# Kernel optimization log

Measured on AMD Instinct MI355X. Metric: run time of the kernel, lower is better.

## Reference

```python
import jax, jax.numpy as jnp
import numpy as np
from jax import lax

# Static hyperparameters of preprocess_proposals (typical BARON config values)
SHAPE_RATIO_THR = 0.25
AREA_RATIO_THR = 0.01
OBJECTNESS_THR = 0.85
NMS_THR = 0.3
EPS_UNION = 1e-6   # mmdet bbox_overlaps eps
EPS_RATIO = 1e-12
IMG_SIZE = 1024.0
N = 8192


def setup_inputs() -> dict:
    key = jax.random.key(0)
    k1, k2, k3 = jax.random.split(key, 3)
    # realistic proposals inside a 1024x1024 image
    centers = jax.random.uniform(k1, (N, 2), minval=0.0, maxval=IMG_SIZE)
    wh = jax.random.uniform(k2, (N, 2), minval=16.0, maxval=512.0)
    x1y1 = jnp.clip(centers - wh / 2, 0.0, IMG_SIZE)
    x2y2 = jnp.clip(centers + wh / 2, 0.0, IMG_SIZE)
    proposal_boxes = jnp.concatenate([x1y1, x2y2], axis=-1).astype(jnp.float32)
    proposal_scores = jax.random.uniform(k3, (N,), dtype=jnp.float32)
    image_boxes = jnp.array([[0.0, 0.0, IMG_SIZE, IMG_SIZE]], dtype=jnp.float32)
    return {"proposal_boxes": proposal_boxes,
            "proposal_scores": proposal_scores,
            "image_boxes": image_boxes}


def _pairwise_iou(boxes):
    # boxes: [N,4] xyxy -> [N,N] IoU
    area = (boxes[:, 2] - boxes[:, 0]) * (boxes[:, 3] - boxes[:, 1])
    lt = jnp.maximum(boxes[:, None, :2], boxes[None, :, :2])   # [N,N,2]
    rb = jnp.minimum(boxes[:, None, 2:4], boxes[None, :, 2:4])  # [N,N,2]
    wh = jnp.clip(rb - lt, 0.0)
    inter = wh[..., 0] * wh[..., 1]
    union = area[:, None] + area[None, :] - inter
    return inter / jnp.maximum(union, EPS_UNION)


def reference(proposal_boxes, proposal_scores, image_boxes):
    n = proposal_boxes.shape[0]
    img = image_boxes[0]

    # --- IoF(image_box, proposals): intersection / area(image_box) (mmdet 'iof') ---
    lt = jnp.maximum(img[:2], proposal_boxes[:, :2])
    rb = jnp.minimum(img[2:4], proposal_boxes[:, 2:4])
    wh = jnp.clip(rb - lt, 0.0)
    inter = wh[:, 0] * wh[:, 1]
    img_area = (img[2] - img[0]) * (img[3] - img[1])
    iofs = inter / jnp.maximum(img_area, EPS_UNION)

    # --- shape-ratio / area / objectness filters ---
    sizes = proposal_boxes[:, 2:4] - proposal_boxes[:, :2]
    shape_ratio = sizes[:, 0] / (sizes[:, 1] + EPS_RATIO)
    valid_shape_ratio = (shape_ratio > SHAPE_RATIO_THR) & (shape_ratio < 1.0 / SHAPE_RATIO_THR)
    valid = valid_shape_ratio & (iofs > AREA_RATIO_THR) & (proposal_scores > OBJECTNESS_THR)
    # fallback: if nothing survives, keep only the highest-scoring proposal
    valid = jnp.where(valid.any(),
                      valid,
                      jnp.arange(n) == jnp.argmax(proposal_scores))

    # --- NMS on the valid subset (invalid boxes never kept, never suppress) ---
    order = jnp.argsort(-proposal_scores)   # score-descending, as torchvision nms
    b = proposal_boxes[order]
    s = proposal_scores[order]
    v = valid[order]

    iou = lax.stop_gradient(_pairwise_iou(b))  # [N,N] suppression pattern is non-diff
    idx = jnp.arange(n)

    def body(i, keep):
        suppress = (iou[i] > NMS_THR) & (idx > i)
        return jnp.where(keep[i], keep & ~suppress, keep)

    keep = lax.fori_loop(0, n, body, v)

    # fixed-shape output: [N,5] = (x1,y1,x2,y2,score), zeroed where pruned,
    # sorted by descending score; keep mask returned alongside.
    out = jnp.concatenate([b, s[:, None]], axis=-1) * keep[:, None].astype(b.dtype)
    return out, keep
```

## Files before the change

### kernel.cpp

```cpp
#include <hip/hip_runtime.h>

#define NPROP 8192
#define NT 1024
typedef unsigned long long u64;

__device__ __forceinline__ int bucket_of(float s) {
    int b = (int)(s * 8192.0f);
    return b < 0 ? 0 : (b > NPROP - 1 ? NPROP - 1 : b);
}

__device__ __forceinline__ bool iou_gt_thr(float4 a, float4 b) {
    float areaA = (a.z - a.x) * (a.w - a.y);
    float areaB = (b.z - b.x) * (b.w - b.y);
    float lx = fmaxf(a.x, b.x), ly = fmaxf(a.y, b.y);
    float rx = fminf(a.z, b.z), ry = fminf(a.w, b.w);
    float w = fmaxf(rx - lx, 0.0f), h = fmaxf(ry - ly, 0.0f);
    float inter = w * h;
    float uni = areaA + areaB - inter;
    float iou = inter / fmaxf(uni, 1e-6f);
    return iou > 0.3f;
}

__global__ __launch_bounds__(256)
void k_valid(const float* __restrict__ boxes, const float* __restrict__ scores,
             const float* __restrict__ img, unsigned char* __restrict__ vbyte) {
    int i = blockIdx.x * 256 + threadIdx.x;
    float4 bx = reinterpret_cast<const float4*>(boxes)[i];
    float s = scores[i];
    float ix1 = img[0], iy1 = img[1], ix2 = img[2], iy2 = img[3];
    float img_area = (ix2 - ix1) * (iy2 - iy1);
    float w = bx.z - bx.x, h = bx.w - bx.y;
    float ratio = w / (h + 1e-12f);
    bool vs = (ratio > 0.25f) && (ratio < 4.0f);
    float lx = fmaxf(ix1, bx.x), ly = fmaxf(iy1, bx.y);
    float rx = fminf(ix2, bx.z), ry = fminf(iy2, bx.w);
    float iw = fmaxf(rx - lx, 0.0f), ih = fmaxf(ry - ly, 0.0f);
    float iof = (iw * ih) / fmaxf(img_area, 1e-6f);
    vbyte[i] = (vs && (iof > 0.01f) && (s > 0.85f)) ? 1 : 0;
}

__global__ __launch_bounds__(NT)
void k_sort1(const float* __restrict__ scores, const unsigned char* __restrict__ vbyte,
             unsigned* __restrict__ prefP, int* __restrict__ tmp_idx,
             int* __restrict__ meta) {
    __shared__ int hist[NPROP];
    __shared__ int wsum[16], wexcl[16];
    const int tid = threadIdx.x, lane = tid & 63, wave = tid >> 6;
    #pragma unroll
    for (int u = 0; u < 8; u++) hist[tid * 8 + u] = 0;
    __syncthreads();
    const float4* s4 = reinterpret_cast<const float4*>(scores);
    float4 sa = s4[tid * 2], sb = s4[tid * 2 + 1];
    float ss[8] = {sa.x, sa.y, sa.z, sa.w, sb.x, sb.y, sb.z, sb.w};
    u64 vb8 = reinterpret_cast<const u64*>(vbyte)[tid];
    int bk[8], vf[8];
    #pragma unroll
    for (int u = 0; u < 8; u++) {
        bk[u] = bucket_of(ss[u]);
        vf[u] = (int)((vb8 >> (8 * u)) & 1ull);
        atomicAdd(&hist[bk[u]], 1 + (vf[u] << 16));
    }
    __syncthreads();
    int h[8]; int tot = 0;
    #pragma unroll
    for (int u = 0; u < 8; u++) { h[u] = hist[tid * 8 + u]; tot += h[u]; }
    int incl = tot;
    #pragma unroll
    for (int off = 1; off < 64; off <<= 1) {
        int n = __shfl_up(incl, off, 64);
        if (lane >= off) incl += n;
    }
    if (lane == 63) wsum[wave] = incl;
    __syncthreads();
    if (tid == 0) {
        int acc = 0;
        #pragma unroll
        for (int w = 0; w < 16; w++) { int t = wsum[w]; wexcl[w] = acc; acc += t; }
        int Vraw = acc >> 16;
        int V = Vraw == 0 ? 1 : Vraw;
        meta[0] = V;
        meta[1] = (V + 63) >> 6;
        meta[2] = Vraw;
    }
    __syncthreads();
    int run = wexcl[wave] + (incl - tot);
    int runA = run & 0xffff;
    #pragma unroll
    for (int u = 0; u < 8; u++) { prefP[tid * 8 + u] = (unsigned)run; run += h[u]; }
    __syncthreads();
    #pragma unroll
    for (int u = 0; u < 8; u++) { hist[tid * 8 + u] = runA; runA += h[u] & 0xffff; }
    __syncthreads();
    #pragma unroll
    for (int u = 0; u < 8; u++) {
        int slot = atomicAdd(&hist[bk[u]], 1);
        tmp_idx[slot] = (tid * 8 + u) | (vf[u] << 31);
    }
}

__global__ void k_rank(const float* __restrict__ scores, const float* __restrict__ boxes,
                       const int* __restrict__ tmp_idx, const unsigned* __restrict__ prefP,
                       const int* __restrict__ meta,
                       float4* __restrict__ srt_box, float* __restrict__ srt_s,
                       int* __restrict__ crank, float4* __restrict__ cbox) {
    int p = blockIdx.x * blockDim.x + threadIdx.x;
    int ip = tmp_idx[p];
    int i = ip & 0xffff;
    bool vf = ip < 0;
    float s = scores[i];
    u64 key = ((u64)__float_as_uint(s) << 32) | (u64)(unsigned)(NPROP - 1 - i);
    int b = bucket_of(s);
    unsigned pb = prefP[b];
    int lo = (int)(pb & 0xffffu), vlo = (int)(pb >> 16);
    int hi = (b < NPROP - 1) ? (int)(prefP[b + 1] & 0xffffu) : NPROP;
    int cnt = 0, vcnt = 0;
    for (int q = lo; q < hi; q++) {
        int jp = tmp_idx[q];
        int j = jp & 0xffff;
        int vfj = (int)((unsigned)jp >> 31);
        u64 kj = ((u64)__float_as_uint(scores[j]) << 32) | (u64)(unsigned)(NPROP - 1 - j);
        int less = (kj < key) ? 1 : 0;
        cnt += less; vcnt += less & vfj;
    }
    int rank = NPROP - 1 - (lo + cnt);
    float4 bx = reinterpret_cast<const float4*>(boxes)[i];
    srt_box[rank] = bx;
    srt_s[rank] = s;
    int Vraw = meta[2];
    if (vf) {
        int cpos = Vraw - 1 - (vlo + vcnt);
        crank[rank] = cpos;
        cbox[cpos] = bx;
    } else {
        crank[rank] = -1;
    }
    if (Vraw == 0 && rank == 0) { crank[0] = 0; cbox[0] = bx; }
}

__global__ __launch_bounds__(256)
void k_mask(const float4* __restrict__ cbox, const int* __restrict__ meta,
            u64* __restrict__ mask) {
    const int V = meta[0], W = meta[1];
    const int VP = W << 6;
    const int lane = threadIdx.x & 63;
    int gw = blockIdx.x * 4 + (threadIdx.x >> 6);
    for (int r = gw; r < V; r += 1024) {
        float4 br = cbox[r];
        for (int w = (r >> 6); w < W; w++) {
            int col = w * 64 + lane;
            bool ok = (col < V) && (col > r) && iou_gt_thr(br, cbox[col]);
            u64 bal = __ballot(ok);
            if (lane == 0) mask[(u64)w * VP + r] = bal;
        }
    }
}

__global__ __launch_bounds__(NT)
void k_resolve(const u64* __restrict__ mask, const int* __restrict__ meta,
               u64* __restrict__ remG) {
    __shared__ u64 rem[NPROP / 64];
    __shared__ u64 diagb[2][64];
    __shared__ u64 nextw[64];
    __shared__ u64 pullw[2];
    __shared__ int klidx[NPROP];
    __shared__ int Ksh;
    const int V = meta[0], W = meta[1];
    const int VP = W << 6;
    const int tid = threadIdx.x, lane = tid & 63, wave = tid >> 6;

    for (int w = tid; w < NPROP / 64; w += NT) {
        int b0 = w * 64; u64 m;
        if (b0 >= V) m = ~0ull;
        else if (b0 + 64 <= V) m = 0ull;
        else m = (~0ull) << (V - b0);
        rem[w] = m;
    }
    if (tid == 0) { Ksh = 0; pullw[0] = 0; pullw[1] = 0; }
    if (wave == 15) diagb[0][lane] = (lane < V) ? mask[lane] : 0ull;
    __syncthreads();

    for (int b = 0; b < W; b++) {
        const int rb0 = b << 6;
        const int nb = b + 1;
        const int K = Ksh;
        u64 keptb = 0;
        if (wave == 0) {
            u64 d = diagb[b & 1][lane];
            int dlo = (int)(unsigned)(d & 0xffffffffull);
            int dhi = (int)(unsigned)(d >> 32);
            u64 r0 = rem[b] | pullw[b & 1];
            unsigned rl_ = (unsigned)__builtin_amdgcn_readfirstlane((int)(unsigned)(r0 & 0xffffffffull));
            unsigned rh_ = (unsigned)__builtin_amdgcn_readfirstlane((int)(unsigned)(r0 >> 32));
            u64 r = ((u64)rh_ << 32) | (u64)rl_;
            u64 avail = ~r;
            while (avail) {
                int i = (int)__builtin_ctzll(avail);
                unsigned xl = (unsigned)__builtin_amdgcn_readlane(dlo, i);
                unsigned xh = (unsigned)__builtin_amdgcn_readlane(dhi, i);
                u64 di = ((u64)xh << 32) | (u64)xl;
                r |= di;
                u64 x = avail & ~di;
                avail = x & (x - 1);
            }
            keptb = ~r;
            if (lane == 0) rem[b] = r;
        } else if (wave <= 13) {
            if (nb < W) {
                u64 myor = 0;
                for (int t = (wave - 1) * 64 + lane; t < K; t += 13 * 64)
                    myor |= mask[(u64)nb * VP + klidx[t]];
                #pragma unroll
                for (int off = 1; off < 64; off <<= 1)
                    myor |= __shfl_xor(myor, off, 64);
                if (lane == 0 && myor)
                    atomicOr((unsigned long long*)&pullw[nb & 1], myor);
            }
        } else if (wave == 14) {
            if (nb < W) {
                int r_ = rb0 + lane;
                nextw[lane] = (r_ < V) ? mask[(u64)nb * VP + r_] : 0ull;
            }
        } else {
            if (nb < W) {
                int r_ = (nb << 6) + lane;
                diagb[nb & 1][lane] = (r_ < V) ? mask[(u64)nb * VP + r_] : 0ull;
            }
        }
        __syncthreads();
        if (wave == 0) {
            if (nb < W) {
                u64 t = ((keptb >> lane) & 1ull) ? nextw[lane] : 0ull;
                #pragma unroll
                for (int off = 1; off < 64; off <<= 1)
                    t |= __shfl_xor(t, off, 64);
                if (lane == 0 && t)
                    atomicOr((unsigned long long*)&pullw[nb & 1], t);
            }
            if ((keptb >> lane) & 1ull) {
                int pos = (int)__popcll(keptb & ((1ull << lane) - 1ull));
                klidx[K + pos] = rb0 + lane;
            }
            if (lane == 0) Ksh = K + (int)__popcll(keptb);
        } else if (tid == 64) {
            pullw[b & 1] = 0;
        }
        __syncthreads();
    }

    for (int w = tid; w < NPROP / 64; w += NT) remG[w] = rem[w];
}

__global__ __launch_bounds__(256)
void k_out(const float4* __restrict__ srt_box, const float* __restrict__ srt_s,
           const int* __restrict__ crank, const u64* __restrict__ remG,
           float* __restrict__ out) {
    int tid = blockIdx.x * 256 + threadIdx.x;
    float ob[20]; float om[4];
    #pragma unroll
    for (int u = 0; u < 4; u++) {
        int p = tid * 4 + u;
        float4 b = srt_box[p];
        float s = srt_s[p];
        int k = crank[p];
        bool keep = (k >= 0) && !((remG[k >> 6] >> (k & 63)) & 1ull);
        float m = keep ? 1.0f : 0.0f;
        ob[u * 5 + 0] = b.x * m;
        ob[u * 5 + 1] = b.y * m;
        ob[u * 5 + 2] = b.z * m;
        ob[u * 5 + 3] = b.w * m;
        ob[u * 5 + 4] = s * m;
        om[u] = m;
    }
    float4* o4 = reinterpret_cast<float4*>(out) + tid * 5;
    #pragma unroll
    for (int q = 0; q < 5; q++)
        o4[q] = make_float4(ob[q * 4 + 0], ob[q * 4 + 1], ob[q * 4 + 2], ob[q * 4 + 3]);
    reinterpret_cast<float4*>(out + NPROP * 5)[tid] =
        make_float4(om[0], om[1], om[2], om[3]);
}

extern "C" void kernel_launch(void* const* d_in, const int* in_sizes, int n_in,
                              void* d_out, int out_size, void* d_ws, size_t ws_size,
                              hipStream_t stream) {
    const float* boxes  = (const float*)d_in[0];
    const float* scores = (const float*)d_in[1];
    const float* img    = (const float*)d_in[2];
    char* ws = (char*)d_ws;
    unsigned* prefP  = (unsigned*)(ws + 0);
    int*    tmp_idx  = (int*)(ws + 32768);
    unsigned char* vbyte = (unsigned char*)(ws + 65536);
    float*  srt_s    = (float*)(ws + 73728);
    float4* srt_box  = (float4*)(ws + 106496);
    float4* cbox     = (float4*)(ws + 237568);
    int*    crank    = (int*)(ws + 368640);
    int*    meta     = (int*)(ws + 401408);
    u64*    remG     = (u64*)(ws + 402432);
    u64*    mask     = (u64*)(ws + 403456);
    float* out = (float*)d_out;

    k_valid<<<32, 256, 0, stream>>>(boxes, scores, img, vbyte);
    k_sort1<<<1, NT, 0, stream>>>(scores, vbyte, prefP, tmp_idx, meta);
    k_rank<<<32, 256, 0, stream>>>(scores, boxes, tmp_idx, prefP, meta,
                                   srt_box, srt_s, crank, cbox);
    k_mask<<<256, 256, 0, stream>>>(cbox, meta, mask);
    k_resolve<<<1, NT, 0, stream>>>(mask, meta, remG);
    k_out<<<8, 256, 0, stream>>>(srt_box, srt_s, crank, remG, out);
}
```

Before: 49.06 us.

## Fuse NMS pipeline into one cooperative kernel with grid syncs

Merges the six separate kernels (validity, bucket sort, rank, mask, resolve, output) into a single cooperative kernel of 8 blocks, using grid-wide syncs instead of kernel boundaries. The aim is to remove per-launch overhead and inter-kernel gaps that dominate a small pipeline. In exchange, the mask-building stage now runs on only 8 blocks instead of 256, and each grid.sync has its own cost. The histogram is now built with global atomics across blocks. The old multi-kernel path stays as a fallback if the cooperative launch fails.

After: 100.1 us. 2.04x slower.

```diff
diff --git a/kernel.cpp b/kernel.cpp
--- a/kernel.cpp
+++ b/kernel.cpp
@@ -1,6 +1,10 @@
 #include <hip/hip_runtime.h>
+#include <hip/hip_cooperative_groups.h>
+
+namespace cg = cooperative_groups;
 
 #define NPROP 8192
+#define NBLK 8
 #define NT 1024
 typedef unsigned long long u64;
 
@@ -19,6 +23,250 @@
     float uni = areaA + areaB - inter;
     float iou = inter / fmaxf(uni, 1e-6f);
     return iou > 0.3f;
+}
+
+__global__ __launch_bounds__(NT)
+void k_mega(const float* __restrict__ boxes, const float* __restrict__ scores,
+            const float* __restrict__ img,
+            int* hist, unsigned* prefP, int* tmp_idx, unsigned char* vbyte,
+            float* srt_s, float4* srt_box, float4* cbox, int* crank,
+            int* meta, u64* remG, u64* mask, float* out) {
+    cg::grid_group grid = cg::this_grid();
+    __shared__ int wsum[16], wexcl[16];
+    __shared__ u64 rem[NPROP / 64];
+    __shared__ u64 diagb[2][64];
+    __shared__ u64 nextw[64];
+    __shared__ u64 pullw[2];
+    __shared__ int klidx[NPROP];
+    __shared__ int Ksh;
+
+    const int tid = threadIdx.x, lane = tid & 63, wave = tid >> 6;
+    const int GT = blockIdx.x * NT + tid;
+
+    {
+        float4 bx = reinterpret_cast<const float4*>(boxes)[GT];
+        float s = scores[GT];
+        float ix1 = img[0], iy1 = img[1], ix2 = img[2], iy2 = img[3];
+        float img_area = (ix2 - ix1) * (iy2 - iy1);
+        float w = bx.z - bx.x, h = bx.w - bx.y;
+        float ratio = w / (h + 1e-12f);
+        bool vs = (ratio > 0.25f) && (ratio < 4.0f);
+        float lx = fmaxf(ix1, bx.x), ly = fmaxf(iy1, bx.y);
+        float rx = fminf(ix2, bx.z), ry = fminf(iy2, bx.w);
+        float iw = fmaxf(rx - lx, 0.0f), ih = fmaxf(ry - ly, 0.0f);
+        float iof = (iw * ih) / fmaxf(img_area, 1e-6f);
+        vbyte[GT] = (vs && (iof > 0.01f) && (s > 0.85f)) ? 1 : 0;
+        hist[GT] = 0;
+    }
+    grid.sync();
+
+    {
+        float s = scores[GT];
+        int vf = (int)vbyte[GT];
+        atomicAdd(&hist[bucket_of(s)], 1 + (vf << 16));
+    }
+    grid.sync();
+
+    if (blockIdx.x == 0) {
+        int h[8]; int tot = 0;
+        #pragma unroll
+        for (int u = 0; u < 8; u++) { h[u] = hist[tid * 8 + u]; tot += h[u]; }
+        int incl = tot;
+        #pragma unroll
+        for (int off = 1; off < 64; off <<= 1) {
+            int n = __shfl_up(incl, off, 64);
+            if (lane >= off) incl += n;
+        }
+        if (lane == 63) wsum[wave] = incl;
+        __syncthreads();
+        if (tid == 0) {
+            int acc = 0;
+            #pragma unroll
+            for (int w = 0; w < 16; w++) { int t = wsum[w]; wexcl[w] = acc; acc += t; }
+            int Vraw = acc >> 16;
+            int V = Vraw == 0 ? 1 : Vraw;
+            meta[0] = V;
+            meta[1] = (V + 63) >> 6;
+            meta[2] = Vraw;
+        }
+        __syncthreads();
+        int run = wexcl[wave] + (incl - tot);
+        int runA = run & 0xffff;
+        #pragma unroll
+        for (int u = 0; u < 8; u++) { prefP[tid * 8 + u] = (unsigned)run; run += h[u]; }
+        #pragma unroll
+        for (int u = 0; u < 8; u++) { hist[tid * 8 + u] = runA; runA += h[u] & 0xffff; }
+    }
+    grid.sync();
+
+    {
+        float s = scores[GT];
+        int vf = (int)vbyte[GT];
+        int slot = atomicAdd(&hist[bucket_of(s)], 1);
+        tmp_idx[slot] = GT | (vf << 31);
+    }
+    grid.sync();
+
+    {
+        int ip = tmp_idx[GT];
+        int i = ip & 0xffff;
+        bool vf = ip < 0;
+        float s = scores[i];
+        u64 key = ((u64)__float_as_uint(s) << 32) | (u64)(unsigned)(NPROP - 1 - i);
+        int b = bucket_of(s);
+        unsigned pb = prefP[b];
+        int lo = (int)(pb & 0xffffu), vlo = (int)(pb >> 16);
+        int hi = (b < NPROP - 1) ? (int)(prefP[b + 1] & 0xffffu) : NPROP;
+        int cnt2 = 0, vcnt = 0;
+        for (int q = lo; q < hi; q++) {
+            int jp = tmp_idx[q];
+            int j = jp & 0xffff;
+            int vfj = (int)((unsigned)jp >> 31);
+            u64 kj = ((u64)__float_as_uint(scores[j]) << 32) | (u64)(unsigned)(NPROP - 1 - j);
+            int less = (kj < key) ? 1 : 0;
+            cnt2 += less; vcnt += less & vfj;
+        }
+        int rank = NPROP - 1 - (lo + cnt2);
+        float4 bx = reinterpret_cast<const float4*>(boxes)[i];
+        srt_box[rank] = bx;
+        srt_s[rank] = s;
+        int Vraw = meta[2];
+        if (vf) {
+            int cpos = Vraw - 1 - (vlo + vcnt);
+            crank[rank] = cpos;
+            cbox[cpos] = bx;
+        } else {
+            crank[rank] = -1;
+        }
+        if (Vraw == 0 && rank == 0) { crank[0] = 0; cbox[0] = bx; }
+    }
+    grid.sync();
+
+    {
+        const int V = meta[0], W = meta[1];
+        const int VP = W << 6;
+        int gw = blockIdx.x * 16 + wave;
+        for (int r = gw; r < V; r += NBLK * 16) {
+            float4 br = cbox[r];
+            for (int w = (r >> 6); w < W; w++) {
+                int col = w * 64 + lane;
+                bool ok = (col < V) && (col > r) && iou_gt_thr(br, cbox[col]);
+                u64 bal = __ballot(ok);
+                if (lane == 0) mask[(u64)w * VP + r] = bal;
+            }
+        }
+    }
+    grid.sync();
+
+    if (blockIdx.x == 0) {
+        const int V = meta[0], W = meta[1];
+        const int VP = W << 6;
+        for (int w = tid; w < NPROP / 64; w += NT) {
+            int b0 = w * 64; u64 m;
+            if (b0 >= V) m = ~0ull;
+            else if (b0 + 64 <= V) m = 0ull;
+            else m = (~0ull) << (V - b0);
+            rem[w] = m;
+        }
+        if (tid == 0) { Ksh = 0; pullw[0] = 0; pullw[1] = 0; }
+        if (wave == 15) diagb[0][lane] = (lane < V) ? mask[lane] : 0ull;
+        __syncthreads();
+
+        for (int b = 0; b < W; b++) {
+            const int rb0 = b << 6;
+            const int nb = b + 1;
+            const int K = Ksh;
+            u64 keptb = 0;
+            if (wave == 0) {
+                u64 d = diagb[b & 1][lane];
+                int dlo = (int)(unsigned)(d & 0xffffffffull);
+                int dhi = (int)(unsigned)(d >> 32);
+                u64 r0 = rem[b] | pullw[b & 1];
+                unsigned rl_ = (unsigned)__builtin_amdgcn_readfirstlane((int)(unsigned)(r0 & 0xffffffffull));
+                unsigned rh_ = (unsigned)__builtin_amdgcn_readfirstlane((int)(unsigned)(r0 >> 32));
+                u64 r = ((u64)rh_ << 32) | (u64)rl_;
+                u64 avail = ~r;
+                while (avail) {
+                    int i = (int)__builtin_ctzll(avail);
+                    unsigned xl = (unsigned)__builtin_amdgcn_readlane(dlo, i);
+                    unsigned xh = (unsigned)__builtin_amdgcn_readlane(dhi, i);
+                    u64 di = ((u64)xh << 32) | (u64)xl;
+                    r |= di;
+                    u64 x = avail & ~di;
+                    avail = x & (x - 1);
+                }
+                keptb = ~r;
+                if (lane == 0) rem[b] = r;
+            } else if (wave <= 13) {
+                if (nb < W) {
+                    u64 myor = 0;
+                    for (int t = (wave - 1) * 64 + lane; t < K; t += 13 * 64)
+                        myor |= mask[(u64)nb * VP + klidx[t]];
+                    #pragma unroll
+                    for (int off = 1; off < 64; off <<= 1)
+                        myor |= __shfl_xor(myor, off, 64);
+                    if (lane == 0 && myor)
+                        atomicOr((unsigned long long*)&pullw[nb & 1], myor);
+                }
+            } else if (wave == 14) {
+                if (nb < W) {
+                    int r_ = rb0 + lane;
+                    nextw[lane] = (r_ < V) ? mask[(u64)nb * VP + r_] : 0ull;
+                }
+            } else {
+                if (nb < W) {
+                    int r_ = (nb << 6) + lane;
+                    diagb[nb & 1][lane] = (r_ < V) ? mask[(u64)nb * VP + r_] : 0ull;
+                }
+            }
+            __syncthreads();
+            if (wave == 0) {
+                if (nb < W) {
+                    u64 t = ((keptb >> lane) & 1ull) ? nextw[lane] : 0ull;
+                    #pragma unroll
+                    for (int off = 1; off < 64; off <<= 1)
+                        t |= __shfl_xor(t, off, 64);
+                    if (lane == 0 && t)
+                        atomicOr((unsigned long long*)&pullw[nb & 1], t);
+                }
+                if ((keptb >> lane) & 1ull) {
+                    int pos = (int)__popcll(keptb & ((1ull << lane) - 1ull));
+                    klidx[K + pos] = rb0 + lane;
+                }
+                if (lane == 0) Ksh = K + (int)__popcll(keptb);
+            } else if (tid == 64) {
+                pullw[b & 1] = 0;
+            }
+            __syncthreads();
+        }
+        for (int w = tid; w < NPROP / 64; w += NT) remG[w] = rem[w];
+    }
+    grid.sync();
+
+    if (GT < 2048) {
+        float ob[20]; float om[4];
+        #pragma unroll
+        for (int u = 0; u < 4; u++) {
+            int p = GT * 4 + u;
+            float4 b = srt_box[p];
+            float s = srt_s[p];
+            int k = crank[p];
+            bool keep = (k >= 0) && !((remG[k >> 6] >> (k & 63)) & 1ull);
+            float m = keep ? 1.0f : 0.0f;
+            ob[u * 5 + 0] = b.x * m;
+            ob[u * 5 + 1] = b.y * m;
+            ob[u * 5 + 2] = b.z * m;
+            ob[u * 5 + 3] = b.w * m;
+            ob[u * 5 + 4] = s * m;
+            om[u] = m;
+        }
+        float4* o4 = reinterpret_cast<float4*>(out) + GT * 5;
+        #pragma unroll
+        for (int q = 0; q < 5; q++)
+            o4[q] = make_float4(ob[q * 4 + 0], ob[q * 4 + 1], ob[q * 4 + 2], ob[q * 4 + 3]);
+        reinterpret_cast<float4*>(out + NPROP * 5)[GT] =
+            make_float4(om[0], om[1], om[2], om[3]);
+    }
 }
 
 __global__ __launch_bounds__(256)
@@ -286,23 +534,32 @@
     const float* scores = (const float*)d_in[1];
     const float* img    = (const float*)d_in[2];
     char* ws = (char*)d_ws;
-    unsigned* prefP  = (unsigned*)(ws + 0);
-    int*    tmp_idx  = (int*)(ws + 32768);
-    unsigned char* vbyte = (unsigned char*)(ws + 65536);
-    float*  srt_s    = (float*)(ws + 73728);
-    float4* srt_box  = (float4*)(ws + 106496);
-    float4* cbox     = (float4*)(ws + 237568);
-    int*    crank    = (int*)(ws + 368640);
-    int*    meta     = (int*)(ws + 401408);
-    u64*    remG     = (u64*)(ws + 402432);
-    u64*    mask     = (u64*)(ws + 403456);
+    int*    hist     = (int*)(ws + 0);
+    unsigned* prefP  = (unsigned*)(ws + 32768);
+    int*    tmp_idx  = (int*)(ws + 65536);
+    unsigned char* vbyte = (unsigned char*)(ws + 98304);
+    float*  srt_s    = (float*)(ws + 106496);
+    float4* srt_box  = (float4*)(ws + 139264);
+    float4* cbox     = (float4*)(ws + 270336);
+    int*    crank    = (int*)(ws + 401408);
+    int*    meta     = (int*)(ws + 434176);
+    u64*    remG     = (u64*)(ws + 435200);
+    u64*    mask     = (u64*)(ws + 436224);
     float* out = (float*)d_out;
 
-    k_valid<<<32, 256, 0, stream>>>(boxes, scores, img, vbyte);
-    k_sort1<<<1, NT, 0, stream>>>(scores, vbyte, prefP, tmp_idx, meta);
-    k_rank<<<32, 256, 0, stream>>>(scores, boxes, tmp_idx, prefP, meta,
-                                   srt_box, srt_s, crank, cbox);
-    k_mask<<<256, 256, 0, stream>>>(cbox, meta, mask);
-    k_resolve<<<1, NT, 0, stream>>>(mask, meta, remG);
-    k_out<<<8, 256, 0, stream>>>(srt_box, srt_s, crank, remG, out);
-}
+    void* args[] = { (void*)&boxes, (void*)&scores, (void*)&img,
+                     (void*)&hist, (void*)&prefP, (void*)&tmp_idx, (void*)&vbyte,
+                     (void*)&srt_s, (void*)&srt_box, (void*)&cbox, (void*)&crank,
+                     (void*)&meta, (void*)&remG, (void*)&mask, (void*)&out };
+    hipError_t err = hipLaunchCooperativeKernel((void*)k_mega, dim3(NBLK), dim3(NT),
+                                                args, 0, stream);
+    if (err != hipSuccess) {
+        k_valid<<<32, 256, 0, stream>>>(boxes, scores, img, vbyte);
+        k_sort1<<<1, NT, 0, stream>>>(scores, vbyte, prefP, tmp_idx, meta);
+        k_rank<<<32, 256, 0, stream>>>(scores, boxes, tmp_idx, prefP, meta,
+                                       srt_box, srt_s, crank, cbox);
+        k_mask<<<256, 256, 0, stream>>>(cbox, meta, mask);
+        k_resolve<<<1, NT, 0, stream>>>(mask, meta, remG);
+        k_out<<<8, 256, 0, stream>>>(srt_box, srt_s, crank, remG, out);
+    }
+}
```

## Fuse validity filter into sort and output scatter into NMS resolve

Applied to the files above, without the earlier changes.

Removes the separate validity kernel by computing the filter flags inside the single-block histogram sort, and removes the final output kernel by zeroing the output in the mask kernel and having the resolve kernel scatter kept boxes by their sorted rank. Only valid proposals now carry box, score and rank data, so the full sorted-box arrays are no longer written. This cuts two launches and some global traffic. In exchange the single-block resolve kernel does the scattered output writes serially, and the sort kernel does more per-thread work.

Measured after the change: 44.46 us, median of 2. -9.4%, faster.

```diff
diff --git a/kernel.cpp b/kernel.cpp
--- a/kernel.cpp
+++ b/kernel.cpp
@@ -21,26 +21,9 @@
     return iou > 0.3f;
 }
 
-__global__ __launch_bounds__(256)
-void k_valid(const float* __restrict__ boxes, const float* __restrict__ scores,
-             const float* __restrict__ img, unsigned char* __restrict__ vbyte) {
-    int i = blockIdx.x * 256 + threadIdx.x;
-    float4 bx = reinterpret_cast<const float4*>(boxes)[i];
-    float s = scores[i];
-    float ix1 = img[0], iy1 = img[1], ix2 = img[2], iy2 = img[3];
-    float img_area = (ix2 - ix1) * (iy2 - iy1);
-    float w = bx.z - bx.x, h = bx.w - bx.y;
-    float ratio = w / (h + 1e-12f);
-    bool vs = (ratio > 0.25f) && (ratio < 4.0f);
-    float lx = fmaxf(ix1, bx.x), ly = fmaxf(iy1, bx.y);
-    float rx = fminf(ix2, bx.z), ry = fminf(iy2, bx.w);
-    float iw = fmaxf(rx - lx, 0.0f), ih = fmaxf(ry - ly, 0.0f);
-    float iof = (iw * ih) / fmaxf(img_area, 1e-6f);
-    vbyte[i] = (vs && (iof > 0.01f) && (s > 0.85f)) ? 1 : 0;
-}
-
 __global__ __launch_bounds__(NT)
-void k_sort1(const float* __restrict__ scores, const unsigned char* __restrict__ vbyte,
+void k_sort1(const float* __restrict__ boxes, const float* __restrict__ scores,
+             const float* __restrict__ img,
              unsigned* __restrict__ prefP, int* __restrict__ tmp_idx,
              int* __restrict__ meta) {
     __shared__ int hist[NPROP];
@@ -49,15 +32,25 @@
     #pragma unroll
     for (int u = 0; u < 8; u++) hist[tid * 8 + u] = 0;
     __syncthreads();
-    const float4* s4 = reinterpret_cast<const float4*>(scores);
-    float4 sa = s4[tid * 2], sb = s4[tid * 2 + 1];
-    float ss[8] = {sa.x, sa.y, sa.z, sa.w, sb.x, sb.y, sb.z, sb.w};
-    u64 vb8 = reinterpret_cast<const u64*>(vbyte)[tid];
-    int bk[8], vf[8];
+    float ix1 = img[0], iy1 = img[1], ix2 = img[2], iy2 = img[3];
+    float img_area = (ix2 - ix1) * (iy2 - iy1);
+    float ss[8]; int pp[8], bk[8], vf[8];
     #pragma unroll
     for (int u = 0; u < 8; u++) {
-        bk[u] = bucket_of(ss[u]);
-        vf[u] = (int)((vb8 >> (8 * u)) & 1ull);
+        int p = u * NT + tid;
+        pp[u] = p;
+        float s = scores[p];
+        float4 bx = reinterpret_cast<const float4*>(boxes)[p];
+        float w = bx.z - bx.x, h = bx.w - bx.y;
+        float ratio = w / (h + 1e-12f);
+        bool vs = (ratio > 0.25f) && (ratio < 4.0f);
+        float lx = fmaxf(ix1, bx.x), ly = fmaxf(iy1, bx.y);
+        float rx = fminf(ix2, bx.z), ry = fminf(iy2, bx.w);
+        float iw = fmaxf(rx - lx, 0.0f), ih = fmaxf(ry - ly, 0.0f);
+        float iof = (iw * ih) / fmaxf(img_area, 1e-6f);
+        ss[u] = s;
+        bk[u] = bucket_of(s);
+        vf[u] = (vs && (iof > 0.01f) && (s > 0.85f)) ? 1 : 0;
         atomicAdd(&hist[bk[u]], 1 + (vf[u] << 16));
     }
     __syncthreads();
@@ -94,19 +87,20 @@
     #pragma unroll
     for (int u = 0; u < 8; u++) {
         int slot = atomicAdd(&hist[bk[u]], 1);
-        tmp_idx[slot] = (tid * 8 + u) | (vf[u] << 31);
+        tmp_idx[slot] = pp[u] | (vf[u] << 31);
     }
 }
 
 __global__ void k_rank(const float* __restrict__ scores, const float* __restrict__ boxes,
                        const int* __restrict__ tmp_idx, const unsigned* __restrict__ prefP,
                        const int* __restrict__ meta,
-                       float4* __restrict__ srt_box, float* __restrict__ srt_s,
-                       int* __restrict__ crank, float4* __restrict__ cbox) {
+                       float4* __restrict__ cbox, float* __restrict__ cscore,
+                       int* __restrict__ vrank) {
     int p = blockIdx.x * blockDim.x + threadIdx.x;
     int ip = tmp_idx[p];
     int i = ip & 0xffff;
     bool vf = ip < 0;
+    int Vraw = meta[2];
     float s = scores[i];
     u64 key = ((u64)__float_as_uint(s) << 32) | (u64)(unsigned)(NPROP - 1 - i);
     int b = bucket_of(s);
@@ -123,23 +117,26 @@
         cnt += less; vcnt += less & vfj;
     }
     int rank = NPROP - 1 - (lo + cnt);
-    float4 bx = reinterpret_cast<const float4*>(boxes)[i];
-    srt_box[rank] = bx;
-    srt_s[rank] = s;
-    int Vraw = meta[2];
     if (vf) {
         int cpos = Vraw - 1 - (vlo + vcnt);
-        crank[rank] = cpos;
+        float4 bx = reinterpret_cast<const float4*>(boxes)[i];
         cbox[cpos] = bx;
-    } else {
-        crank[rank] = -1;
-    }
-    if (Vraw == 0 && rank == 0) { crank[0] = 0; cbox[0] = bx; }
+        cscore[cpos] = s;
+        vrank[cpos] = rank;
+    } else if (Vraw == 0 && rank == 0) {
+        float4 bx = reinterpret_cast<const float4*>(boxes)[i];
+        cbox[0] = bx;
+        cscore[0] = s;
+        vrank[0] = 0;
+    }
 }
 
 __global__ __launch_bounds__(256)
 void k_mask(const float4* __restrict__ cbox, const int* __restrict__ meta,
-            u64* __restrict__ mask) {
+            u64* __restrict__ mask, float* __restrict__ out) {
+    int gid = blockIdx.x * 256 + threadIdx.x;
+    if (gid < (NPROP * 6) / 4)
+        reinterpret_cast<float4*>(out)[gid] = make_float4(0.f, 0.f, 0.f, 0.f);
     const int V = meta[0], W = meta[1];
     const int VP = W << 6;
     const int lane = threadIdx.x & 63;
@@ -157,7 +154,8 @@
 
 __global__ __launch_bounds__(NT)
 void k_resolve(const u64* __restrict__ mask, const int* __restrict__ meta,
-               u64* __restrict__ remG) {
+               const float4* __restrict__ cbox, const float* __restrict__ cscore,
+               const int* __restrict__ vrank, float* __restrict__ out) {
     __shared__ u64 rem[NPROP / 64];
     __shared__ u64 diagb[2][64];
     __shared__ u64 nextw[64];
@@ -247,36 +245,19 @@
         __syncthreads();
     }
 
-    for (int w = tid; w < NPROP / 64; w += NT) remG[w] = rem[w];
-}
-
-__global__ __launch_bounds__(256)
-void k_out(const float4* __restrict__ srt_box, const float* __restrict__ srt_s,
-           const int* __restrict__ crank, const u64* __restrict__ remG,
-           float* __restrict__ out) {
-    int tid = blockIdx.x * 256 + threadIdx.x;
-    float ob[20]; float om[4];
-    #pragma unroll
-    for (int u = 0; u < 4; u++) {
-        int p = tid * 4 + u;
-        float4 b = srt_box[p];
-        float s = srt_s[p];
-        int k = crank[p];
-        bool keep = (k >= 0) && !((remG[k >> 6] >> (k & 63)) & 1ull);
-        float m = keep ? 1.0f : 0.0f;
-        ob[u * 5 + 0] = b.x * m;
-        ob[u * 5 + 1] = b.y * m;
-        ob[u * 5 + 2] = b.z * m;
-        ob[u * 5 + 3] = b.w * m;
-        ob[u * 5 + 4] = s * m;
-        om[u] = m;
-    }
-    float4* o4 = reinterpret_cast<float4*>(out) + tid * 5;
-    #pragma unroll
-    for (int q = 0; q < 5; q++)
-        o4[q] = make_float4(ob[q * 4 + 0], ob[q * 4 + 1], ob[q * 4 + 2], ob[q * 4 + 3]);
-    reinterpret_cast<float4*>(out + NPROP * 5)[tid] =
-        make_float4(om[0], om[1], om[2], om[3]);
+    for (int k = tid; k < V; k += NT) {
+        bool keep = !((rem[k >> 6] >> (k & 63)) & 1ull);
+        if (keep) {
+            int rk = vrank[k];
+            float4 b = cbox[k];
+            out[rk * 5 + 0] = b.x;
+            out[rk * 5 + 1] = b.y;
+            out[rk * 5 + 2] = b.z;
+            out[rk * 5 + 3] = b.w;
+            out[rk * 5 + 4] = cscore[k];
+            out[NPROP * 5 + rk] = 1.0f;
+        }
+    }
 }
 
 extern "C" void kernel_launch(void* const* d_in, const int* in_sizes, int n_in,
@@ -288,21 +269,16 @@
     char* ws = (char*)d_ws;
     unsigned* prefP  = (unsigned*)(ws + 0);
     int*    tmp_idx  = (int*)(ws + 32768);
-    unsigned char* vbyte = (unsigned char*)(ws + 65536);
-    float*  srt_s    = (float*)(ws + 73728);
-    float4* srt_box  = (float4*)(ws + 106496);
-    float4* cbox     = (float4*)(ws + 237568);
-    int*    crank    = (int*)(ws + 368640);
-    int*    meta     = (int*)(ws + 401408);
-    u64*    remG     = (u64*)(ws + 402432);
-    u64*    mask     = (u64*)(ws + 403456);
+    float*  cscore   = (float*)(ws + 65536);
+    float4* cbox     = (float4*)(ws + 98304);
+    int*    vrank    = (int*)(ws + 229376);
+    int*    meta     = (int*)(ws + 262144);
+    u64*    mask     = (u64*)(ws + 263168);
     float* out = (float*)d_out;
 
-    k_valid<<<32, 256, 0, stream>>>(boxes, scores, img, vbyte);
-    k_sort1<<<1, NT, 0, stream>>>(scores, vbyte, prefP, tmp_idx, meta);
+    k_sort1<<<1, NT, 0, stream>>>(boxes, scores, img, prefP, tmp_idx, meta);
     k_rank<<<32, 256, 0, stream>>>(scores, boxes, tmp_idx, prefP, meta,
-                                   srt_box, srt_s, crank, cbox);
-    k_mask<<<256, 256, 0, stream>>>(cbox, meta, mask);
-    k_resolve<<<1, NT, 0, stream>>>(mask, meta, remG);
-    k_out<<<8, 256, 0, stream>>>(srt_box, srt_s, crank, remG, out);
-}
+                                   cbox, cscore, vrank);
+    k_mask<<<256, 256, 0, stream>>>(cbox, meta, mask, out);
+    k_resolve<<<1, NT, 0, stream>>>(mask, meta, cbox, cscore, vrank, out);
+}
```
